# Kernel tuning notes

Hardware: AMD Instinct MI355X
Metric: run time of the kernel (lower is better)

## Reference

```python
import jax, jax.numpy as jnp
import numpy as np

D, H, NL, DFF, VS, VT = 512, 8, 6, 2048, 32000, 32000
B, SS, ST = 4, 512, 512
PAD = 1
EPS = 1e-5


def _pos_encoding(S, d):
    pos = jnp.arange(S, dtype=jnp.float32)[:, None]
    div = jnp.exp(jnp.arange(0, d, 2, dtype=jnp.float32) * (-jnp.log(jnp.float32(10000.0)) / d))
    pe = jnp.zeros((S, d), dtype=jnp.float32)
    pe = pe.at[:, 0::2].set(jnp.sin(pos * div))
    pe = pe.at[:, 1::2].set(jnp.cos(pos * div))
    return pe


def _ln(x, g, b):
    m = jnp.mean(x, axis=-1, keepdims=True)
    v = jnp.mean(jnp.square(x - m), axis=-1, keepdims=True)
    return (x - m) * jax.lax.rsqrt(v + EPS) * g + b


def _mha(q, k, v, Wq, Wk, Wv, Wo, mask):
    # q,k,v: [B,S,D]; W*: [D,D] (torch Linear: y = x @ W.T); mask True -> masked
    Bq, Sq, _ = q.shape
    Sk = k.shape[1]
    dk = D // H
    Q = (q @ Wq.T).reshape(Bq, Sq, H, dk).transpose(0, 2, 1, 3)
    K = (k @ Wk.T).reshape(Bq, Sk, H, dk).transpose(0, 2, 1, 3)
    V = (v @ Wv.T).reshape(Bq, Sk, H, dk).transpose(0, 2, 1, 3)
    scores = jnp.einsum('bhqd,bhkd->bhqk', Q, K) / jnp.sqrt(jnp.float32(dk))
    scores = jnp.where(mask, -jnp.inf, scores)
    w = jax.nn.softmax(scores, axis=-1)
    w = jnp.nan_to_num(w)  # matches torch.nan_to_num after softmax of all -inf rows
    out = jnp.einsum('bhqk,bhkd->bhqd', w, V)
    out = out.transpose(0, 2, 1, 3).reshape(Bq, Sq, D)
    return out @ Wo.T


def _ffn(x, w1, b1, w2, b2):
    return jax.nn.relu(x @ w1.T + b1) @ w2.T + b2


def setup_inputs() -> dict:
    key = jax.random.key(0)
    ks = jax.random.split(key, 48)
    i = iter(range(48))
    n = lambda shape, s=0.02: jax.random.normal(ks[next(i)], shape, dtype=jnp.float32) * s
    inp = {
        'src': jax.random.randint(ks[next(i)], (B, SS), 0, VS),
        'tgt': jax.random.randint(ks[next(i)], (B, ST), 0, VT),
        'src_embed': n((VS, D)),
        'tgt_embed': n((VT, D)),
        'enc_Wq': n((NL, D, D)), 'enc_Wk': n((NL, D, D)), 'enc_Wv': n((NL, D, D)), 'enc_Wo': n((NL, D, D)),
        'enc_w1': n((NL, DFF, D)), 'enc_b1': jnp.zeros((NL, DFF)),
        'enc_w2': n((NL, D, DFF)), 'enc_b2': jnp.zeros((NL, D)),
        'enc_ln1g': jnp.ones((NL, D)), 'enc_ln1b': jnp.zeros((NL, D)),
        'enc_ln2g': jnp.ones((NL, D)), 'enc_ln2b': jnp.zeros((NL, D)),
        'enc_lnfg': jnp.ones((D,)), 'enc_lnfb': jnp.zeros((D,)),
        'dec_sWq': n((NL, D, D)), 'dec_sWk': n((NL, D, D)), 'dec_sWv': n((NL, D, D)), 'dec_sWo': n((NL, D, D)),
        'dec_cWq': n((NL, D, D)), 'dec_cWk': n((NL, D, D)), 'dec_cWv': n((NL, D, D)), 'dec_cWo': n((NL, D, D)),
        'dec_w1': n((NL, DFF, D)), 'dec_b1': jnp.zeros((NL, DFF)),
        'dec_w2': n((NL, D, DFF)), 'dec_b2': jnp.zeros((NL, D)),
        'dec_ln1g': jnp.ones((NL, D)), 'dec_ln1b': jnp.zeros((NL, D)),
        'dec_ln2g': jnp.ones((NL, D)), 'dec_ln2b': jnp.zeros((NL, D)),
        'dec_ln3g': jnp.ones((NL, D)), 'dec_ln3b': jnp.zeros((NL, D)),
        'dec_lnfg': jnp.ones((D,)), 'dec_lnfb': jnp.zeros((D,)),
        'out_W': n((VT, D)), 'out_b': jnp.zeros((VT,)),
    }
    return inp


def reference(src, tgt, src_embed, tgt_embed,
              enc_Wq, enc_Wk, enc_Wv, enc_Wo, enc_w1, enc_b1, enc_w2, enc_b2,
              enc_ln1g, enc_ln1b, enc_ln2g, enc_ln2b, enc_lnfg, enc_lnfb,
              dec_sWq, dec_sWk, dec_sWv, dec_sWo, dec_cWq, dec_cWk, dec_cWv, dec_cWo,
              dec_w1, dec_b1, dec_w2, dec_b2,
              dec_ln1g, dec_ln1b, dec_ln2g, dec_ln2b, dec_ln3g, dec_ln3b,
              dec_lnfg, dec_lnfb, out_W, out_b):
    scale = jnp.sqrt(jnp.float32(D))
    src_mask = (src == PAD)[:, None, None, :]                      # [B,1,1,SS]
    causal = jnp.triu(jnp.ones((ST, ST), dtype=bool), k=1)[None, None]
    tgt_mask = (tgt == PAD)[:, None, None, :] | causal             # [B,1,ST,ST]

    # Encoder
    x = src_embed[src] * scale + _pos_encoding(SS, D)[None]
    for l in range(NL):
        nrm = _ln(x, enc_ln1g[l], enc_ln1b[l])
        x = x + _mha(nrm, nrm, nrm, enc_Wq[l], enc_Wk[l], enc_Wv[l], enc_Wo[l], src_mask)
        x = x + _ffn(_ln(x, enc_ln2g[l], enc_ln2b[l]), enc_w1[l], enc_b1[l], enc_w2[l], enc_b2[l])
    memory = _ln(x, enc_lnfg, enc_lnfb)

    # Decoder
    y = tgt_embed[tgt] * scale + _pos_encoding(ST, D)[None]
    for l in range(NL):
        nrm = _ln(y, dec_ln1g[l], dec_ln1b[l])
        y = y + _mha(nrm, nrm, nrm, dec_sWq[l], dec_sWk[l], dec_sWv[l], dec_sWo[l], tgt_mask)
        nrm = _ln(y, dec_ln2g[l], dec_ln2b[l])
        y = y + _mha(nrm, memory, memory, dec_cWq[l], dec_cWk[l], dec_cWv[l], dec_cWo[l], src_mask)
        y = y + _ffn(_ln(y, dec_ln3g[l], dec_ln3b[l]), dec_w1[l], dec_b1[l], dec_w2[l], dec_b2[l])
    y = _ln(y, dec_lnfg, dec_lnfb)

    logits = y @ out_W.T + out_b                                   # [B,ST,VT]
    return logits
```

## Files before the change

kernel.cpp:

```cpp
#include <hip/hip_runtime.h>
#include <hip/hip_bf16.h>
#include <math.h>

#define Dm    512
#define Hh    8
#define NLay  6
#define DFFm  2048
#define Bb    4
#define NTOK  2048
#define PADID 1
#define LNEPS 1e-5f
#define S2W   262144

typedef __attribute__((ext_vector_type(8))) short short8;
typedef __attribute__((ext_vector_type(4))) float f32x4;
typedef unsigned short u16;

__device__ __forceinline__ u16 f2bf(float f) {
    union { float f; unsigned int i; } x; x.f = f;
    unsigned int r = x.i + 0x7fffu + ((x.i >> 16) & 1u);
    return (u16)(r >> 16);
}

typedef const __attribute__((address_space(1))) void* as1cv;
typedef __attribute__((address_space(3))) void* as3v;
__device__ __forceinline__ void gl_lds16(const u16* g, u16* l) {
    __builtin_amdgcn_global_load_lds((as1cv)g, (as3v)l, 16, 0, 0);
}

#define SYNC_VM(N) do { \
    asm volatile("s_waitcnt vmcnt(" #N ")" ::: "memory"); \
    __builtin_amdgcn_s_barrier(); \
    __builtin_amdgcn_sched_barrier(0); \
} while (0)

__device__ __forceinline__ void swz_tile(int& mt, int& nt) {
    const int nwg  = gridDim.x * gridDim.y;
    const int orig = blockIdx.y * gridDim.x + blockIdx.x;
    const int q8 = nwg >> 3, r8 = nwg & 7;
    const int xcd = orig & 7, idx = orig >> 3;
    const int wgid = (xcd < r8 ? xcd * (q8 + 1) : r8 * (q8 + 1) + (xcd - r8) * q8) + idx;
    const int MT = gridDim.y;
    mt = wgid % MT;
    nt = wgid / MT;
}

struct CvtJobs {
    const float* s[17];
    u16*         d[17];
    long         n4[17];
};
__global__ __launch_bounds__(256) void cvt_many(CvtJobs j) {
    const int job = blockIdx.y;
    const long n4 = j.n4[job];
    const float* in = j.s[job];
    u16* out = j.d[job];
    long i = (long)blockIdx.x * 256 + threadIdx.x;
    const long stride = (long)gridDim.x * 256;
    for (; i < n4; i += stride) {
        float4 v = ((const float4*)in)[i];
        ushort4 o;
        o.x = f2bf(v.x); o.y = f2bf(v.y); o.z = f2bf(v.z); o.w = f2bf(v.w);
        ((ushort4*)out)[i] = o;
    }
}

__global__ __launch_bounds__(256) void gemm_bt(
    const u16* __restrict__ A0, const u16* __restrict__ A1,
    const u16* __restrict__ A2, int lda,
    const u16* __restrict__ B0, const u16* __restrict__ B1,
    const u16* __restrict__ B2, int ldb,
    float* Cf, u16* Cb, int csm,
    const float* __restrict__ bias, int relu,
    int Kc, int ns, int vth, int koff, u16* vtp)
{
    __shared__ u16 As[2][4096];
    __shared__ u16 Bs[2][4096];
    int mt, nt; swz_tile(mt, nt);
    const int m0 = mt << 6, n0 = nt << 6;
    const int t = threadIdx.x, lane = t & 63, wave = t >> 6;
    const int wr = (wave >> 1) << 5, wc = (wave & 1) << 5;
    const int fr = lane & 15, fq = lane >> 4;
    const int srow = t >> 3;
    const int sch  = (t & 7) ^ (srow & 7);

    const int p = n0 >> 9;
    const u16* Amat = (p == 0) ? A0 : (p == 1 ? A1 : A2);
    const u16* Bmat; int nb;
    if (B1) { Bmat = (p == 0) ? B0 : (p == 1 ? B1 : B2); nb = n0 & 511; }
    else    { Bmat = B0; nb = n0; }
    const long kb = (long)blockIdx.z * Kc;

    const u16* Ag0 = Amat + (long)(m0 + srow) * lda + kb + (sch << 3);
    const u16* Ag1 = Ag0 + 32L * lda;
    const u16* Bg0 = Bmat + (long)(nb + srow) * ldb + kb + (sch << 3);
    const u16* Bg1 = Bg0 + 32L * ldb;

    f32x4 acc[2][2];
    #pragma unroll
    for (int i = 0; i < 2; i++)
        #pragma unroll
        for (int j = 0; j < 2; j++) acc[i][j] = (f32x4){0.f, 0.f, 0.f, 0.f};

    const int nk = Kc >> 6;
    gl_lds16(Ag0, &As[0][t << 3]);
    gl_lds16(Ag1, &As[0][(t + 256) << 3]);
    gl_lds16(Bg0, &Bs[0][t << 3]);
    gl_lds16(Bg1, &Bs[0][(t + 256) << 3]);
    __syncthreads();
    for (int ki = 0; ki < nk; ki++) {
        const int cur = ki & 1;
        if (ki + 1 < nk) {
            const int ko = (ki + 1) << 6;
            gl_lds16(Ag0 + ko, &As[cur ^ 1][t << 3]);
            gl_lds16(Ag1 + ko, &As[cur ^ 1][(t + 256) << 3]);
            gl_lds16(Bg0 + ko, &Bs[cur ^ 1][t << 3]);
            gl_lds16(Bg1 + ko, &Bs[cur ^ 1][(t + 256) << 3]);
        }
        const int r0 = wr + fr, r1 = wr + 16 + fr;
        const int c0 = wc + fr, c1 = wc + 16 + fr;
        #pragma unroll
        for (int h = 0; h < 2; h++) {
            const int lc = fq | (h << 2);
            short8 af0 = *(const short8*)&As[cur][(r0 << 6) + ((lc ^ (r0 & 7)) << 3)];
            short8 af1 = *(const short8*)&As[cur][(r1 << 6) + ((lc ^ (r1 & 7)) << 3)];
            short8 bf0 = *(const short8*)&Bs[cur][(c0 << 6) + ((lc ^ (c0 & 7)) << 3)];
            short8 bf1 = *(const short8*)&Bs[cur][(c1 << 6) + ((lc ^ (c1 & 7)) << 3)];
            acc[0][0] = __builtin_amdgcn_mfma_f32_16x16x32_bf16(af0, bf0, acc[0][0], 0, 0, 0);
            acc[0][1] = __builtin_amdgcn_mfma_f32_16x16x32_bf16(af0, bf1, acc[0][1], 0, 0, 0);
            acc[1][0] = __builtin_amdgcn_mfma_f32_16x16x32_bf16(af1, bf0, acc[1][0], 0, 0, 0);
            acc[1][1] = __builtin_amdgcn_mfma_f32_16x16x32_bf16(af1, bf1, acc[1][1], 0, 0, 0);
        }
        __syncthreads();
    }

    #pragma unroll
    for (int i = 0; i < 2; i++) {
        #pragma unroll
        for (int j = 0; j < 2; j++) {
            const int nl  = n0 + wc + (j << 4) + fr;
            const int mlb = m0 + wr + (i << 4) + (fq << 2);
            const float bsv = bias ? bias[nl] : 0.f;
            #pragma unroll
            for (int r = 0; r < 4; r++) {
                const int ml = mlb + r;
                if (ns > 1) {
                    float v = acc[i][j][r] + (blockIdx.z == 0 ? bsv : 0.f);
                    unsafeAtomicAdd(&Cf[(long)ml * csm + nl + koff], v);
                } else {
                    float v = acc[i][j][r] + bsv;
                    if (nl >= vth) {
                        vtp[(long)(ml >> 9) * S2W + (long)(nl - vth) * 512 + (ml & 511)] = f2bf(v);
                    } else {
                        if (relu) v = fmaxf(v, 0.f);
                        long ci = (long)ml * csm + nl + koff;
                        if (Cf) Cf[ci] = v;
                        if (Cb) Cb[ci] = f2bf(v);
                    }
                }
            }
        }
    }
}

__global__ __launch_bounds__(256) void gemm_kv6(
    const u16* __restrict__ A,
    const u16* __restrict__ Wk, const u16* __restrict__ Wv,
    u16* __restrict__ kc, u16* __restrict__ vtc)
{
    __shared__ u16 As[2][4096];
    __shared__ u16 Bs[2][4096];
    int mt, nt; swz_tile(mt, nt);
    const int m0 = mt << 6, n0 = nt << 6;
    const int z = blockIdx.z;
    const int t = threadIdx.x, lane = t & 63, wave = t >> 6;
    const int wr = (wave >> 1) << 5, wc = (wave & 1) << 5;
    const int fr = lane & 15, fq = lane >> 4;
    const int srow = t >> 3;
    const int sch  = (t & 7) ^ (srow & 7);

    const int p = n0 >> 9;
    const u16* Bmat = ((p == 0) ? Wk : Wv) + (size_t)z * S2W;
    const int nb = n0 & 511;

    const u16* Ag0 = A + (long)(m0 + srow) * 512 + (sch << 3);
    const u16* Ag1 = Ag0 + 32L * 512;
    const u16* Bg0 = Bmat + (long)(nb + srow) * 512 + (sch << 3);
    const u16* Bg1 = Bg0 + 32L * 512;

    f32x4 acc[2][2];
    #pragma unroll
    for (int i = 0; i < 2; i++)
        #pragma unroll
        for (int j = 0; j < 2; j++) acc[i][j] = (f32x4){0.f, 0.f, 0.f, 0.f};

    gl_lds16(Ag0, &As[0][t << 3]);
    gl_lds16(Ag1, &As[0][(t + 256) << 3]);
    gl_lds16(Bg0, &Bs[0][t << 3]);
    gl_lds16(Bg1, &Bs[0][(t + 256) << 3]);
    __syncthreads();
    for (int ki = 0; ki < 8; ki++) {
        const int cur = ki & 1;
        if (ki + 1 < 8) {
            const int ko = (ki + 1) << 6;
            gl_lds16(Ag0 + ko, &As[cur ^ 1][t << 3]);
            gl_lds16(Ag1 + ko, &As[cur ^ 1][(t + 256) << 3]);
            gl_lds16(Bg0 + ko, &Bs[cur ^ 1][t << 3]);
            gl_lds16(Bg1 + ko, &Bs[cur ^ 1][(t + 256) << 3]);
        }
        const int r0 = wr + fr, r1 = wr + 16 + fr;
        const int c0 = wc + fr, c1 = wc + 16 + fr;
        #pragma unroll
        for (int h = 0; h < 2; h++) {
            const int lc = fq | (h << 2);
            short8 af0 = *(const short8*)&As[cur][(r0 << 6) + ((lc ^ (r0 & 7)) << 3)];
            short8 af1 = *(const short8*)&As[cur][(r1 << 6) + ((lc ^ (r1 & 7)) << 3)];
            short8 bf0 = *(const short8*)&Bs[cur][(c0 << 6) + ((lc ^ (c0 & 7)) << 3)];
            short8 bf1 = *(const short8*)&Bs[cur][(c1 << 6) + ((lc ^ (c1 & 7)) << 3)];
            acc[0][0] = __builtin_amdgcn_mfma_f32_16x16x32_bf16(af0, bf0, acc[0][0], 0, 0, 0);
            acc[0][1] = __builtin_amdgcn_mfma_f32_16x16x32_bf16(af0, bf1, acc[0][1], 0, 0, 0);
            acc[1][0] = __builtin_amdgcn_mfma_f32_16x16x32_bf16(af1, bf0, acc[1][0], 0, 0, 0);
            acc[1][1] = __builtin_amdgcn_mfma_f32_16x16x32_bf16(af1, bf1, acc[1][1], 0, 0, 0);
        }
        __syncthreads();
    }

    #pragma unroll
    for (int i = 0; i < 2; i++) {
        #pragma unroll
        for (int j = 0; j < 2; j++) {
            const int nl  = n0 + wc + (j << 4) + fr;
            const int mlb = m0 + wr + (i << 4) + (fq << 2);
            #pragma unroll
            for (int r = 0; r < 4; r++) {
                const int ml = mlb + r;
                const u16 v = f2bf(acc[i][j][r]);
                if (nl < 512)
                    kc[(long)z * NTOK * 512 + (long)ml * 512 + nl] = v;
                else
                    vtc[(long)z * Bb * S2W + (long)(ml >> 9) * S2W +
                        (long)(nl - 512) * 512 + (ml & 511)] = v;
            }
        }
    }
}

__global__ __launch_bounds__(256) void gemm_big(
    const u16* __restrict__ A, int lda,
    const u16* __restrict__ B, int ldb,
    float* Cf, int ldc,
    const float* __restrict__ bias, int K)
{
    __shared__ u16 As[3][4096];
    __shared__ u16 Bs[3][4096];
    int mt, nt; swz_tile(mt, nt);
    const int m0 = mt << 7, n0 = nt << 7;
    const int t = threadIdx.x, lane = t & 63, wave = t >> 6;
    const int wr = (wave >> 1) << 6, wc = (wave & 1) << 6;
    const int fr = lane & 15, fq = lane >> 4;
    const int srow = t >> 2;
    const int sch  = (t & 3) ^ ((srow >> 1) & 3);
    const u16* Ag0 = A + (long)(m0 + srow) * lda + (sch << 3);
    const u16* Ag1 = A + (long)(m0 + 64 + srow) * lda + (sch << 3);
    const u16* Bg0 = B + (long)(n0 + srow) * ldb + (sch << 3);
    const u16* Bg1 = B + (long)(n0 + 64 + srow) * ldb + (sch << 3);

    f32x4 acc[4][4];
    #pragma unroll
    for (int i = 0; i < 4; i++)
        #pragma unroll
        for (int j = 0; j < 4; j++) acc[i][j] = (f32x4){0.f, 0.f, 0.f, 0.f};

    const int nk = K >> 5;
    auto stage = [&](int ki, int buf) {
        const int ko = ki << 5;
        gl_lds16(Ag0 + ko, &As[buf][t << 3]);
        gl_lds16(Ag1 + ko, &As[buf][(t + 256) << 3]);
        gl_lds16(Bg0 + ko, &Bs[buf][t << 3]);
        gl_lds16(Bg1 + ko, &Bs[buf][(t + 256) << 3]);
    };
    stage(0, 0);
    if (nk > 1) { stage(1, 1); SYNC_VM(4); }
    else        { SYNC_VM(0); }

    int cur = 0;
    for (int ki = 0; ki < nk; ki++) {
        const bool st = (ki + 2 < nk);
        if (st) stage(ki + 2, cur == 0 ? 2 : cur - 1);
        short8 af[4], bf[4];
        #pragma unroll
        for (int i = 0; i < 4; i++) {
            const int r = wr + (i << 4) + fr;
            af[i] = *(const short8*)&As[cur][(r << 5) + ((fq ^ ((r >> 1) & 3)) << 3)];
        }
        #pragma unroll
        for (int j = 0; j < 4; j++) {
            const int c = wc + (j << 4) + fr;
            bf[j] = *(const short8*)&Bs[cur][(c << 5) + ((fq ^ ((c >> 1) & 3)) << 3)];
        }
        #pragma unroll
        for (int i = 0; i < 4; i++)
            #pragma unroll
            for (int j = 0; j < 4; j++)
                acc[i][j] = __builtin_amdgcn_mfma_f32_16x16x32_bf16(af[i], bf[j], acc[i][j], 0, 0, 0);
        if (ki + 1 < nk) {
            if (st) SYNC_VM(4);
            else    SYNC_VM(0);
        }
        cur = (cur == 2) ? 0 : cur + 1;
    }

    #pragma unroll
    for (int i = 0; i < 4; i++) {
        #pragma unroll
        for (int j = 0; j < 4; j++) {
            const int nl  = n0 + wc + (j << 4) + fr;
            const int mlb = m0 + wr + (i << 4) + (fq << 2);
            const float bsv = bias ? bias[nl] : 0.f;
            #pragma unroll
            for (int r = 0; r < 4; r++)
                Cf[(long)(mlb + r) * ldc + nl] = acc[i][j][r] + bsv;
        }
    }
}

__global__ __launch_bounds__(256) void attn_fused(
    const u16* __restrict__ qkb, const u16* __restrict__ kb_, int ldk,
    const u16* __restrict__ vt,
    const int* __restrict__ ids, u16* __restrict__ attc, int causal)
{
    __shared__ u16 Ks[2][4096];
    __shared__ u16 Vs[2][4096];
    __shared__ short Ps[4][16][72];
    const int t = threadIdx.x, lane = t & 63, w = t >> 6;
    const int fr = lane & 15, fq = lane >> 4;
    const int q0 = blockIdx.x << 6, h = blockIdx.y, b = blockIdx.z;

    const u16* qp = qkb + (long)(b * 512 + q0 + (w << 4) + fr) * 1024 + h * 64 + (fq << 3);
    short8 aq0 = *(const short8*)qp;
    short8 aq1 = *(const short8*)(qp + 32);

    const int sr = t >> 3, sc = (t & 7) ^ (sr & 7);
    const u16* kg0 = kb_ + (long)(b * 512 + sr) * ldk + h * 64 + (sc << 3);
    const u16* kg1 = kg0 + 32L * ldk;
    const u16* vg0 = vt + (long)b * S2W + (long)(h * 64 + sr) * 512 + (sc << 3);
    const u16* vg1 = vg0 + 32L * 512;

    unsigned pmask = 0;
    #pragma unroll
    for (int kt = 0; kt < 8; kt++)
        #pragma unroll
        for (int j = 0; j < 4; j++)
            if (ids[b * 512 + (kt << 6) + (j << 4) + fr] == PADID)
                pmask |= 1u << ((kt << 2) + j);

    float m[4], l[4]; f32x4 oc[4];
    #pragma unroll
    for (int r = 0; r < 4; r++) { m[r] = -INFINITY; l[r] = 0.f; oc[r] = (f32x4){0.f,0.f,0.f,0.f}; }

    const int lastkt = causal ? (q0 >> 6) : 7;
    auto stage = [&](int kt, int buf) {
        const long so = (long)(kt << 6);
        gl_lds16(kg0 + so * ldk, &Ks[buf][t << 3]);
        gl_lds16(kg1 + so * ldk, &Ks[buf][(t + 256) << 3]);
        gl_lds16(vg0 + so, &Vs[buf][t << 3]);
        gl_lds16(vg1 + so, &Vs[buf][(t + 256) << 3]);
    };
    stage(0, 0);
    __syncthreads();

    for (int kt = 0; kt <= lastkt; kt++) {
        const int cur = kt & 1;
        if (kt < lastkt) stage(kt + 1, cur ^ 1);

        f32x4 sc4[4];
        #pragma unroll
        for (int j = 0; j < 4; j++) sc4[j] = (f32x4){0.f,0.f,0.f,0.f};
        #pragma unroll
        for (int j = 0; j < 4; j++) {
            const int rr = (j << 4) + fr;
            short8 bk0 = *(const short8*)&Ks[cur][rr * 64 + ((fq ^ (rr & 7)) << 3)];
            short8 bk1 = *(const short8*)&Ks[cur][rr * 64 + (((fq | 4) ^ (rr & 7)) << 3)];
            sc4[j] = __builtin_amdgcn_mfma_f32_16x16x32_bf16(aq0, bk0, sc4[j], 0, 0, 0);
            sc4[j] = __builtin_amdgcn_mfma_f32_16x16x32_bf16(aq1, bk1, sc4[j], 0, 0, 0);
        }
        const int s0 = kt << 6;
        #pragma unroll
        for (int r = 0; r < 4; r++) {
            const int qa = q0 + (w << 4) + (fq << 2) + r;
            float mx = -INFINITY;
            #pragma unroll
            for (int j = 0; j < 4; j++) {
                bool msk = ((pmask >> ((kt << 2) + j)) & 1) ||
                           (causal && (s0 + (j << 4) + fr) > qa);
                float sv = msk ? -INFINITY : sc4[j][r] * 0.125f;
                sc4[j][r] = sv;
                mx = fmaxf(mx, sv);
            }
            mx = fmaxf(mx, __shfl_xor(mx, 1)); mx = fmaxf(mx, __shfl_xor(mx, 2));
            mx = fmaxf(mx, __shfl_xor(mx, 4)); mx = fmaxf(mx, __shfl_xor(mx, 8));
            float mnew  = fmaxf(m[r], mx);
            float scale = (mnew == -INFINITY) ? 1.f : __expf(m[r] - mnew);
            float ps = 0.f;
            #pragma unroll
            for (int j = 0; j < 4; j++) {
                float p2 = (sc4[j][r] == -INFINITY) ? 0.f : __expf(sc4[j][r] - mnew);
                sc4[j][r] = p2; ps += p2;
            }
            ps += __shfl_xor(ps, 1); ps += __shfl_xor(ps, 2);
            ps += __shfl_xor(ps, 4); ps += __shfl_xor(ps, 8);
            l[r] = l[r] * scale + ps;
            m[r] = mnew;
            #pragma unroll
            for (int j2 = 0; j2 < 4; j2++) oc[j2][r] *= scale;
        }
        #pragma unroll
        for (int r = 0; r < 4; r++)
            #pragma unroll
            for (int j = 0; j < 4; j++)
                Ps[w][(fq << 2) + r][(j << 4) + fr] = (short)f2bf(sc4[j][r]);
        #pragma unroll
        for (int kc2 = 0; kc2 < 2; kc2++) {
            short8 pa = *(const short8*)&Ps[w][fr][(kc2 << 5) + (fq << 3)];
            #pragma unroll
            for (int j2 = 0; j2 < 4; j2++) {
                const int rd = (j2 << 4) + fr;
                const int cch = (((kc2 << 2) | fq) ^ (rd & 7));
                short8 bv = *(const short8*)&Vs[cur][rd * 64 + (cch << 3)];
                oc[j2] = __builtin_amdgcn_mfma_f32_16x16x32_bf16(pa, bv, oc[j2], 0, 0, 0);
            }
        }
        __syncthreads();
    }

    float inv[4];
    #pragma unroll
    for (int r = 0; r < 4; r++) inv[r] = (l[r] > 0.f) ? 1.f / l[r] : 0.f;
    #pragma unroll
    for (int j2 = 0; j2 < 4; j2++)
        #pragma unroll
        for (int r = 0; r < 4; r++)
            attc[(long)(b * 512 + q0 + (w << 4) + (fq << 2) + r) * 512 + h * 64 + (j2 << 4) + fr]
                = f2bf(oc[j2][r] * inv[r]);
}

__global__ __launch_bounds__(256) void ln_rows(
    const float* __restrict__ x, const float* __restrict__ g,
    const float* __restrict__ b, u16* __restrict__ out)
{
    int row  = blockIdx.x * 4 + (threadIdx.x >> 6);
    int lane = threadIdx.x & 63;
    const float* xr = x + (long)row * Dm;
    float v[8]; float s = 0.f;
    #pragma unroll
    for (int i = 0; i < 8; i++) { v[i] = xr[lane + (i << 6)]; s += v[i]; }
    #pragma unroll
    for (int o = 32; o > 0; o >>= 1) s += __shfl_xor(s, o);
    float mean = s * (1.f / 512.f);
    float q = 0.f;
    #pragma unroll
    for (int i = 0; i < 8; i++) { float d = v[i] - mean; q += d * d; }
    #pragma unroll
    for (int o = 32; o > 0; o >>= 1) q += __shfl_xor(q, o);
    float rinv = rsqrtf(q * (1.f / 512.f) + LNEPS);
    u16* orow = out + (long)row * Dm;
    #pragma unroll
    for (int i = 0; i < 8; i++) {
        int c = lane + (i << 6);
        orow[c] = f2bf((v[i] - mean) * rinv * g[c] + b[c]);
    }
}

__global__ __launch_bounds__(256) void embed_pe(
    const int* __restrict__ ids, const float* __restrict__ emb,
    float* __restrict__ out)
{
    int idx = blockIdx.x * 256 + threadIdx.x;
    int d   = idx & 511;
    int tok = idx >> 9;
    int s   = tok & 511;
    int id  = ids[tok];
    float val = emb[(long)id * Dm + d] * 22.62741699796952f;
    int i2 = d >> 1;
    float dv  = expf((float)(i2 << 1) * (-9.210340371976184f / 512.f));
    float ang = (float)s * dv;
    val += (d & 1) ? cosf(ang) : sinf(ang);
    out[idx] = val;
}

extern "C" void kernel_launch(void* const* d_in, const int* in_sizes, int n_in,
                              void* d_out, int out_size, void* d_ws, size_t ws_size,
                              hipStream_t stream)
{
    (void)in_sizes; (void)n_in; (void)out_size; (void)ws_size;
    const int*   src       = (const int*)d_in[0];
    const int*   tgt       = (const int*)d_in[1];
    const float* src_embed = (const float*)d_in[2];
    const float* tgt_embed = (const float*)d_in[3];
    const float* enc_b1  = (const float*)d_in[9];
    const float* enc_b2  = (const float*)d_in[11];
    const float* enc_ln1g = (const float*)d_in[12];
    const float* enc_ln1b = (const float*)d_in[13];
    const float* enc_ln2g = (const float*)d_in[14];
    const float* enc_ln2b = (const float*)d_in[15];
    const float* enc_lnfg = (const float*)d_in[16];
    const float* enc_lnfb = (const float*)d_in[17];
    const float* dec_b1  = (const float*)d_in[27];
    const float* dec_b2  = (const float*)d_in[29];
    const float* dec_ln1g = (const float*)d_in[30];
    const float* dec_ln1b = (const float*)d_in[31];
    const float* dec_ln2g = (const float*)d_in[32];
    const float* dec_ln2b = (const float*)d_in[33];
    const float* dec_ln3g = (const float*)d_in[34];
    const float* dec_ln3b = (const float*)d_in[35];
    const float* dec_lnfg = (const float*)d_in[36];
    const float* dec_lnfb = (const float*)d_in[37];
    const float* out_b  = (const float*)d_in[39];

    char* wp = (char*)d_ws;
    auto carve = [&](size_t nbytes) {
        void* p = (void*)wp; wp += (nbytes + 255) & ~(size_t)255; return p;
    };

    const long nW = (long)NLay * S2W;
    const long nF = (long)NLay * DFFm * Dm;
    const long nO = 32000L * Dm;

    u16* Wb[12];
    for (int i = 0; i < 12; i++) Wb[i] = (u16*)carve((size_t)nW * 2);
    u16* w1E  = (u16*)carve((size_t)nF * 2);
    u16* w2E  = (u16*)carve((size_t)nF * 2);
    u16* w1D  = (u16*)carve((size_t)nF * 2);
    u16* w2D  = (u16*)carve((size_t)nF * 2);
    u16* outW = (u16*)carve((size_t)nO * 2);

    float* x  = (float*)carve((size_t)NTOK * Dm * 4);
    float* y  = (float*)carve((size_t)NTOK * Dm * 4);
    u16* nrm  = (u16*)carve((size_t)NTOK * Dm * 2);
    u16* qkb  = (u16*)carve((size_t)NTOK * 1024 * 2);
    u16* vt   = (u16*)carve((size_t)Bb * Dm * 512 * 2);
    u16* attc = (u16*)carve((size_t)NTOK * Dm * 2);
    u16* h1   = (u16*)carve((size_t)NTOK * DFFm * 2);
    u16* memn = (u16*)carve((size_t)NTOK * Dm * 2);
    u16* kc6  = (u16*)carve((size_t)NLay * NTOK * 512 * 2);
    u16* vt6  = (u16*)carve((size_t)NLay * Bb * S2W * 2);

    const int wi[12] = {4, 5, 6, 7, 18, 19, 20, 21, 22, 23, 24, 25};
    CvtJobs jobs;
    for (int i = 0; i < 12; i++) {
        jobs.s[i] = (const float*)d_in[wi[i]]; jobs.d[i] = Wb[i]; jobs.n4[i] = nW >> 2;
    }
    jobs.s[12] = (const float*)d_in[8];  jobs.d[12] = w1E;  jobs.n4[12] = nF >> 2;
    jobs.s[13] = (const float*)d_in[10]; jobs.d[13] = w2E;  jobs.n4[13] = nF >> 2;
    jobs.s[14] = (const float*)d_in[26]; jobs.d[14] = w1D;  jobs.n4[14] = nF >> 2;
    jobs.s[15] = (const float*)d_in[28]; jobs.d[15] = w2D;  jobs.n4[15] = nF >> 2;
    jobs.s[16] = (const float*)d_in[38]; jobs.d[16] = outW; jobs.n4[16] = nO >> 2;
    cvt_many<<<dim3(512, 17), 256, 0, stream>>>(jobs);

    const int BIG = 1 << 28;
    u16 *eWq = Wb[0], *eWk = Wb[1], *eWv = Wb[2], *eWo = Wb[3];
    u16 *sWq = Wb[4], *sWk = Wb[5], *sWv = Wb[6], *sWo = Wb[7];
    u16 *cWq = Wb[8], *cWk = Wb[9], *cWv = Wb[10], *cWo = Wb[11];

    embed_pe<<<4096, 256, 0, stream>>>(src, src_embed, x);
    for (int l = 0; l < NLay; l++) {
        const size_t wo = (size_t)l * S2W;
        ln_rows<<<512, 256, 0, stream>>>(x, enc_ln1g + l * Dm, enc_ln1b + l * Dm, nrm);
        gemm_bt<<<dim3(24, 32, 1), 256, 0, stream>>>(nrm, nrm, nrm, 512,
            eWq + wo, eWk + wo, eWv + wo, 512,
            nullptr, qkb, 1024, nullptr, 0, 512, 1, 1024, 0, vt);
        attn_fused<<<dim3(8, Hh, Bb), 256, 0, stream>>>(qkb, qkb + 512, 1024, vt, src, attc, 0);
        gemm_bt<<<dim3(8, 32, 4), 256, 0, stream>>>(attc, attc, attc, 512,
            eWo + wo, nullptr, nullptr, 512,
            x, nullptr, 512, nullptr, 0, 128, 4, BIG, 0, nullptr);
        ln_rows<<<512, 256, 0, stream>>>(x, enc_ln2g + l * Dm, enc_ln2b + l * Dm, nrm);
        gemm_bt<<<dim3(32, 32, 1), 256, 0, stream>>>(nrm, nrm, nrm, 512,
            w1E + (size_t)l * DFFm * Dm, nullptr, nullptr, 512,
            nullptr, h1, DFFm, enc_b1 + l * DFFm, 1, 512, 1, BIG, 0, nullptr);
        gemm_bt<<<dim3(8, 32, 4), 256, 0, stream>>>(h1, h1, h1, DFFm,
            w2E + (size_t)l * Dm * DFFm, nullptr, nullptr, DFFm,
            x, nullptr, 512, enc_b2 + l * Dm, 0, 512, 4, BIG, 0, nullptr);
    }
    ln_rows<<<512, 256, 0, stream>>>(x, enc_lnfg, enc_lnfb, memn);
    gemm_kv6<<<dim3(16, 32, NLay), 256, 0, stream>>>(memn, cWk, cWv, kc6, vt6);

    embed_pe<<<4096, 256, 0, stream>>>(tgt, tgt_embed, y);
    for (int l = 0; l < NLay; l++) {
        const size_t wo = (size_t)l * S2W;
        ln_rows<<<512, 256, 0, stream>>>(y, dec_ln1g + l * Dm, dec_ln1b + l * Dm, nrm);
        gemm_bt<<<dim3(24, 32, 1), 256, 0, stream>>>(nrm, nrm, nrm, 512,
            sWq + wo, sWk + wo, sWv + wo, 512,
            nullptr, qkb, 1024, nullptr, 0, 512, 1, 1024, 0, vt);
        attn_fused<<<dim3(8, Hh, Bb), 256, 0, stream>>>(qkb, qkb + 512, 1024, vt, tgt, attc, 1);
        gemm_bt<<<dim3(8, 32, 4), 256, 0, stream>>>(attc, attc, attc, 512,
            sWo + wo, nullptr, nullptr, 512,
            y, nullptr, 512, nullptr, 0, 128, 4, BIG, 0, nullptr);
        ln_rows<<<512, 256, 0, stream>>>(y, dec_ln2g + l * Dm, dec_ln2b + l * Dm, nrm);
        gemm_bt<<<dim3(8, 32, 1), 256, 0, stream>>>(nrm, nrm, nrm, 512,
            cWq + wo, nullptr, nullptr, 512,
            nullptr, qkb, 1024, nullptr, 0, 512, 1, BIG, 0, nullptr);
        attn_fused<<<dim3(8, Hh, Bb), 256, 0, stream>>>(qkb,
            kc6 + (size_t)l * NTOK * 512, 512, vt6 + (size_t)l * Bb * S2W, src, attc, 0);
        gemm_bt<<<dim3(8, 32, 4), 256, 0, stream>>>(attc, attc, attc, 512,
            cWo + wo, nullptr, nullptr, 512,
            y, nullptr, 512, nullptr, 0, 128, 4, BIG, 0, nullptr);
        ln_rows<<<512, 256, 0, stream>>>(y, dec_ln3g + l * Dm, dec_ln3b + l * Dm, nrm);
        gemm_bt<<<dim3(32, 32, 1), 256, 0, stream>>>(nrm, nrm, nrm, 512,
            w1D + (size_t)l * DFFm * Dm, nullptr, nullptr, 512,
            nullptr, h1, DFFm, dec_b1 + l * DFFm, 1, 512, 1, BIG, 0, nullptr);
        gemm_bt<<<dim3(8, 32, 4), 256, 0, stream>>>(h1, h1, h1, DFFm,
            w2D + (size_t)l * Dm * DFFm, nullptr, nullptr, DFFm,
            y, nullptr, 512, dec_b2 + l * Dm, 0, 512, 4, BIG, 0, nullptr);
    }
    ln_rows<<<512, 256, 0, stream>>>(y, dec_lnfg, dec_lnfb, nrm);

    gemm_big<<<dim3(250, 16), 256, 0, stream>>>(nrm, 512, outW, 512,
        (float*)d_out, 32000, out_b, 512);
}
```

Baseline: 1.753 ms.

## Split attention KV range across wave pairs and halve query tile per block

The attention kernel now handles 32 query rows per block instead of 64. The two wave pairs each process half of the key/value tiles, and their partial softmax states (m, l, O) are merged through shared memory at the end. This doubles the grid to give more blocks on the GPU and shortens each block's serial KV loop. The cost is losing the prefetch double buffering, since both buffers now hold different KV halves with a sync each iteration, plus a merge step. Separately, the split-K factor of the Wo projection GEMMs drops from 4 to 2.

```diff
diff --git a/kernel.cpp b/kernel.cpp
--- a/kernel.cpp
+++ b/kernel.cpp
@@ -334,9 +334,10 @@
     __shared__ short Ps[4][16][72];
     const int t = threadIdx.x, lane = t & 63, w = t >> 6;
     const int fr = lane & 15, fq = lane >> 4;
-    const int q0 = blockIdx.x << 6, h = blockIdx.y, b = blockIdx.z;
-
-    const u16* qp = qkb + (long)(b * 512 + q0 + (w << 4) + fr) * 1024 + h * 64 + (fq << 3);
+    const int qh = w & 1, kvh = w >> 1;
+    const int q0 = blockIdx.x << 5, h = blockIdx.y, b = blockIdx.z;
+
+    const u16* qp = qkb + (long)(b * 512 + q0 + (qh << 4) + fr) * 1024 + h * 64 + (fq << 3);
     short8 aq0 = *(const short8*)qp;
     short8 aq1 = *(const short8*)(qp + 32);
 
@@ -354,94 +355,130 @@
             if (ids[b * 512 + (kt << 6) + (j << 4) + fr] == PADID)
                 pmask |= 1u << ((kt << 2) + j);
 
+    const int nkt = causal ? (((q0 + 31) >> 6) + 1) : 8;
+    const int nA = (nkt + 1) >> 1, nB = nkt - nA;
+    const int myn = kvh ? nB : nA;
+
     float m[4], l[4]; f32x4 oc[4];
     #pragma unroll
     for (int r = 0; r < 4; r++) { m[r] = -INFINITY; l[r] = 0.f; oc[r] = (f32x4){0.f,0.f,0.f,0.f}; }
 
-    const int lastkt = causal ? (q0 >> 6) : 7;
-    auto stage = [&](int kt, int buf) {
-        const long so = (long)(kt << 6);
-        gl_lds16(kg0 + so * ldk, &Ks[buf][t << 3]);
-        gl_lds16(kg1 + so * ldk, &Ks[buf][(t + 256) << 3]);
-        gl_lds16(vg0 + so, &Vs[buf][t << 3]);
-        gl_lds16(vg1 + so, &Vs[buf][(t + 256) << 3]);
-    };
-    stage(0, 0);
+    for (int i = 0; i < nA; i++) {
+        {
+            const long soA = (long)(i << 6);
+            gl_lds16(kg0 + soA * ldk, &Ks[0][t << 3]);
+            gl_lds16(kg1 + soA * ldk, &Ks[0][(t + 256) << 3]);
+            gl_lds16(vg0 + soA,       &Vs[0][t << 3]);
+            gl_lds16(vg1 + soA,       &Vs[0][(t + 256) << 3]);
+            if (i < nB) {
+                const long soB = (long)((nA + i) << 6);
+                gl_lds16(kg0 + soB * ldk, &Ks[1][t << 3]);
+                gl_lds16(kg1 + soB * ldk, &Ks[1][(t + 256) << 3]);
+                gl_lds16(vg0 + soB,       &Vs[1][t << 3]);
+                gl_lds16(vg1 + soB,       &Vs[1][(t + 256) << 3]);
+            }
+        }
+        __syncthreads();
+
+        if (i < myn) {
+            const int kt = (kvh ? nA : 0) + i;
+            f32x4 sc4[4];
+            #pragma unroll
+            for (int j = 0; j < 4; j++) sc4[j] = (f32x4){0.f,0.f,0.f,0.f};
+            #pragma unroll
+            for (int j = 0; j < 4; j++) {
+                const int rr = (j << 4) + fr;
+                short8 bk0 = *(const short8*)&Ks[kvh][rr * 64 + ((fq ^ (rr & 7)) << 3)];
+                short8 bk1 = *(const short8*)&Ks[kvh][rr * 64 + (((fq | 4) ^ (rr & 7)) << 3)];
+                sc4[j] = __builtin_amdgcn_mfma_f32_16x16x32_bf16(aq0, bk0, sc4[j], 0, 0, 0);
+                sc4[j] = __builtin_amdgcn_mfma_f32_16x16x32_bf16(aq1, bk1, sc4[j], 0, 0, 0);
+            }
+            const int s0 = kt << 6;
+            #pragma unroll
+            for (int r = 0; r < 4; r++) {
+                const int qa = q0 + (qh << 4) + (fq << 2) + r;
+                float mx = -INFINITY;
+                #pragma unroll
+                for (int j = 0; j < 4; j++) {
+                    bool msk = ((pmask >> ((kt << 2) + j)) & 1) ||
+                               (causal && (s0 + (j << 4) + fr) > qa);
+                    float sv = msk ? -INFINITY : sc4[j][r] * 0.125f;
+                    sc4[j][r] = sv;
+                    mx = fmaxf(mx, sv);
+                }
+                mx = fmaxf(mx, __shfl_xor(mx, 1)); mx = fmaxf(mx, __shfl_xor(mx, 2));
+                mx = fmaxf(mx, __shfl_xor(mx, 4)); mx = fmaxf(mx, __shfl_xor(mx, 8));
+                float mnew  = fmaxf(m[r], mx);
+                float scale = (mnew == -INFINITY) ? 1.f : __expf(m[r] - mnew);
+                float ps = 0.f;
+                #pragma unroll
+                for (int j = 0; j < 4; j++) {
+                    float p2 = (sc4[j][r] == -INFINITY) ? 0.f : __expf(sc4[j][r] - mnew);
+                    sc4[j][r] = p2; ps += p2;
+                }
+                ps += __shfl_xor(ps, 1); ps += __shfl_xor(ps, 2);
+                ps += __shfl_xor(ps, 4); ps += __shfl_xor(ps, 8);
+                l[r] = l[r] * scale + ps;
+                m[r] = mnew;
+                #pragma unroll
+                for (int j2 = 0; j2 < 4; j2++) oc[j2][r] *= scale;
+            }
+            #pragma unroll
+            for (int r = 0; r < 4; r++)
+                #pragma unroll
+                for (int j = 0; j < 4; j++)
+                    Ps[w][(fq << 2) + r][(j << 4) + fr] = (short)f2bf(sc4[j][r]);
+            #pragma unroll
+            for (int kc2 = 0; kc2 < 2; kc2++) {
+                short8 pa = *(const short8*)&Ps[w][fr][(kc2 << 5) + (fq << 3)];
+                #pragma unroll
+                for (int j2 = 0; j2 < 4; j2++) {
+                    const int rd = (j2 << 4) + fr;
+                    const int cch = (((kc2 << 2) | fq) ^ (rd & 7));
+                    short8 bv = *(const short8*)&Vs[kvh][rd * 64 + (cch << 3)];
+                    oc[j2] = __builtin_amdgcn_mfma_f32_16x16x32_bf16(pa, bv, oc[j2], 0, 0, 0);
+                }
+            }
+        }
+        __syncthreads();
+    }
+
+    float* Ob = (float*)&Ks[0][0];
+    float* Ml = (float*)&Vs[0][0];
+    if (kvh == 1) {
+        #pragma unroll
+        for (int r = 0; r < 4; r++) {
+            const int row = (qh << 4) + (fq << 2) + r;
+            Ml[(row << 1)]     = m[r];
+            Ml[(row << 1) + 1] = l[r];
+            #pragma unroll
+            for (int j2 = 0; j2 < 4; j2++)
+                Ob[(row << 6) + (j2 << 4) + fr] = oc[j2][r];
+        }
+    }
     __syncthreads();
-
-    for (int kt = 0; kt <= lastkt; kt++) {
-        const int cur = kt & 1;
-        if (kt < lastkt) stage(kt + 1, cur ^ 1);
-
-        f32x4 sc4[4];
-        #pragma unroll
-        for (int j = 0; j < 4; j++) sc4[j] = (f32x4){0.f,0.f,0.f,0.f};
-        #pragma unroll
-        for (int j = 0; j < 4; j++) {
-            const int rr = (j << 4) + fr;
-            short8 bk0 = *(const short8*)&Ks[cur][rr * 64 + ((fq ^ (rr & 7)) << 3)];
-            short8 bk1 = *(const short8*)&Ks[cur][rr * 64 + (((fq | 4) ^ (rr & 7)) << 3)];
-            sc4[j] = __builtin_amdgcn_mfma_f32_16x16x32_bf16(aq0, bk0, sc4[j], 0, 0, 0);
-            sc4[j] = __builtin_amdgcn_mfma_f32_16x16x32_bf16(aq1, bk1, sc4[j], 0, 0, 0);
-        }
-        const int s0 = kt << 6;
+    if (kvh == 0) {
         #pragma unroll
         for (int r = 0; r < 4; r++) {
-            const int qa = q0 + (w << 4) + (fq << 2) + r;
-            float mx = -INFINITY;
-            #pragma unroll
-            for (int j = 0; j < 4; j++) {
-                bool msk = ((pmask >> ((kt << 2) + j)) & 1) ||
-                           (causal && (s0 + (j << 4) + fr) > qa);
-                float sv = msk ? -INFINITY : sc4[j][r] * 0.125f;
-                sc4[j][r] = sv;
-                mx = fmaxf(mx, sv);
-            }
-            mx = fmaxf(mx, __shfl_xor(mx, 1)); mx = fmaxf(mx, __shfl_xor(mx, 2));
-            mx = fmaxf(mx, __shfl_xor(mx, 4)); mx = fmaxf(mx, __shfl_xor(mx, 8));
-            float mnew  = fmaxf(m[r], mx);
-            float scale = (mnew == -INFINITY) ? 1.f : __expf(m[r] - mnew);
-            float ps = 0.f;
-            #pragma unroll
-            for (int j = 0; j < 4; j++) {
-                float p2 = (sc4[j][r] == -INFINITY) ? 0.f : __expf(sc4[j][r] - mnew);
-                sc4[j][r] = p2; ps += p2;
-            }
-            ps += __shfl_xor(ps, 1); ps += __shfl_xor(ps, 2);
-            ps += __shfl_xor(ps, 4); ps += __shfl_xor(ps, 8);
-            l[r] = l[r] * scale + ps;
-            m[r] = mnew;
-            #pragma unroll
-            for (int j2 = 0; j2 < 4; j2++) oc[j2][r] *= scale;
-        }
-        #pragma unroll
-        for (int r = 0; r < 4; r++)
-            #pragma unroll
-            for (int j = 0; j < 4; j++)
-                Ps[w][(fq << 2) + r][(j << 4) + fr] = (short)f2bf(sc4[j][r]);
-        #pragma unroll
-        for (int kc2 = 0; kc2 < 2; kc2++) {
-            short8 pa = *(const short8*)&Ps[w][fr][(kc2 << 5) + (fq << 3)];
+            const int row = (qh << 4) + (fq << 2) + r;
+            const float mB = Ml[(row << 1)], lB = Ml[(row << 1) + 1];
+            const float mN = fmaxf(m[r], mB);
+            float sA, sB;
+            if (mN == -INFINITY) { sA = 0.f; sB = 0.f; }
+            else {
+                sA = (m[r] == -INFINITY) ? 0.f : __expf(m[r] - mN);
+                sB = (mB   == -INFINITY) ? 0.f : __expf(mB   - mN);
+            }
+            const float L = l[r] * sA + lB * sB;
+            const float inv = (L > 0.f) ? 1.f / L : 0.f;
             #pragma unroll
             for (int j2 = 0; j2 < 4; j2++) {
-                const int rd = (j2 << 4) + fr;
-                const int cch = (((kc2 << 2) | fq) ^ (rd & 7));
-                short8 bv = *(const short8*)&Vs[cur][rd * 64 + (cch << 3)];
-                oc[j2] = __builtin_amdgcn_mfma_f32_16x16x32_bf16(pa, bv, oc[j2], 0, 0, 0);
-            }
-        }
-        __syncthreads();
-    }
-
-    float inv[4];
-    #pragma unroll
-    for (int r = 0; r < 4; r++) inv[r] = (l[r] > 0.f) ? 1.f / l[r] : 0.f;
-    #pragma unroll
-    for (int j2 = 0; j2 < 4; j2++)
-        #pragma unroll
-        for (int r = 0; r < 4; r++)
-            attc[(long)(b * 512 + q0 + (w << 4) + (fq << 2) + r) * 512 + h * 64 + (j2 << 4) + fr]
-                = f2bf(oc[j2][r] * inv[r]);
+                float val = (oc[j2][r] * sA + Ob[(row << 6) + (j2 << 4) + fr] * sB) * inv;
+                attc[(long)(b * 512 + q0 + (qh << 4) + (fq << 2) + r) * 512 +
+                     h * 64 + (j2 << 4) + fr] = f2bf(val);
+            }
+        }
+    }
 }
 
 __global__ __launch_bounds__(256) void ln_rows(
@@ -569,10 +606,10 @@
         gemm_bt<<<dim3(24, 32, 1), 256, 0, stream>>>(nrm, nrm, nrm, 512,
             eWq + wo, eWk + wo, eWv + wo, 512,
             nullptr, qkb, 1024, nullptr, 0, 512, 1, 1024, 0, vt);
-        attn_fused<<<dim3(8, Hh, Bb), 256, 0, stream>>>(qkb, qkb + 512, 1024, vt, src, attc, 0);
-        gemm_bt<<<dim3(8, 32, 4), 256, 0, stream>>>(attc, attc, attc, 512,
+        attn_fused<<<dim3(16, Hh, Bb), 256, 0, stream>>>(qkb, qkb + 512, 1024, vt, src, attc, 0);
+        gemm_bt<<<dim3(8, 32, 2), 256, 0, stream>>>(attc, attc, attc, 512,
             eWo + wo, nullptr, nullptr, 512,
-            x, nullptr, 512, nullptr, 0, 128, 4, BIG, 0, nullptr);
+            x, nullptr, 512, nullptr, 0, 256, 2, BIG, 0, nullptr);
         ln_rows<<<512, 256, 0, stream>>>(x, enc_ln2g + l * Dm, enc_ln2b + l * Dm, nrm);
         gemm_bt<<<dim3(32, 32, 1), 256, 0, stream>>>(nrm, nrm, nrm, 512,
             w1E + (size_t)l * DFFm * Dm, nullptr, nullptr, 512,
@@ -591,19 +628,19 @@
         gemm_bt<<<dim3(24, 32, 1), 256, 0, stream>>>(nrm, nrm, nrm, 512,
             sWq + wo, sWk + wo, sWv + wo, 512,
             nullptr, qkb, 1024, nullptr, 0, 512, 1, 1024, 0, vt);
-        attn_fused<<<dim3(8, Hh, Bb), 256, 0, stream>>>(qkb, qkb + 512, 1024, vt, tgt, attc, 1);
-        gemm_bt<<<dim3(8, 32, 4), 256, 0, stream>>>(attc, attc, attc, 512,
+        attn_fused<<<dim3(16, Hh, Bb), 256, 0, stream>>>(qkb, qkb + 512, 1024, vt, tgt, attc, 1);
+        gemm_bt<<<dim3(8, 32, 2), 256, 0, stream>>>(attc, attc, attc, 512,
             sWo + wo, nullptr, nullptr, 512,
-            y, nullptr, 512, nullptr, 0, 128, 4, BIG, 0, nullptr);
+            y, nullptr, 512, nullptr, 0, 256, 2, BIG, 0, nullptr);
         ln_rows<<<512, 256, 0, stream>>>(y, dec_ln2g + l * Dm, dec_ln2b + l * Dm, nrm);
         gemm_bt<<<dim3(8, 32, 1), 256, 0, stream>>>(nrm, nrm, nrm, 512,
             cWq + wo, nullptr, nullptr, 512,
             nullptr, qkb, 1024, nullptr, 0, 512, 1, BIG, 0, nullptr);
-        attn_fused<<<dim3(8, Hh, Bb), 256, 0, stream>>>(qkb,
+        attn_fused<<<dim3(16, Hh, Bb), 256, 0, stream>>>(qkb,
             kc6 + (size_t)l * NTOK * 512, 512, vt6 + (size_t)l * Bb * S2W, src, attc, 0);
-        gemm_bt<<<dim3(8, 32, 4), 256, 0, stream>>>(attc, attc, attc, 512,
+        gemm_bt<<<dim3(8, 32, 2), 256, 0, stream>>>(attc, attc, attc, 512,
             cWo + wo, nullptr, nullptr, 512,
-            y, nullptr, 512, nullptr, 0, 128, 4, BIG, 0, nullptr);
+            y, nullptr, 512, nullptr, 0, 256, 2, BIG, 0, nullptr);
         ln_rows<<<512, 256, 0, stream>>>(y, dec_ln3g + l * Dm, dec_ln3b + l * Dm, nrm);
         gemm_bt<<<dim3(32, 32, 1), 256, 0, stream>>>(nrm, nrm, nrm, 512,
             w1D + (size_t)l * DFFm * Dm, nullptr, nullptr, 512,
```

New measurement: 1.570 ms. 10.5% less time.
